# Kernel optimization log

Measured on AMD Instinct MI355X. Metric: run time of the kernel, lower is better.

Reference implementation:

```python
import jax, jax.numpy as jnp
import numpy as np

DIM = 768
H = 12          # num query heads
KV = 6          # num kv heads
GS = H // KV    # group size = 2
HD = DIM // H   # head dim = 64


def setup_inputs() -> dict:
    key = jax.random.key(0)
    ks = jax.random.split(key, 6)
    B, P = 8, 1024
    s = DIM ** -0.5
    x = jax.random.normal(ks[0], (B, P, DIM), dtype=jnp.float32)
    Wq = jax.random.normal(ks[1], (DIM, DIM), dtype=jnp.float32) * s
    Wk = jax.random.normal(ks[2], (DIM, KV * HD), dtype=jnp.float32) * s
    Wv = jax.random.normal(ks[3], (DIM, KV * HD), dtype=jnp.float32) * s
    Wp = jax.random.normal(ks[4], (DIM, DIM), dtype=jnp.float32) * s
    bp = jnp.zeros((DIM,), dtype=jnp.float32)
    return {"x": x, "Wq": Wq, "Wk": Wk, "Wv": Wv, "Wp": Wp, "bp": bp}


def reference(x, Wq, Wk, Wv, Wp, bp):
    B, P, C = x.shape
    scale = HD ** -0.5
    # projections; consecutive heads i*GS..(i+1)*GS-1 form kv-group i (torch.split dim=1)
    q = (x @ Wq).reshape(B, P, KV, GS, HD).transpose(0, 2, 3, 1, 4) * scale  # [B,KV,GS,P,d]
    k = (x @ Wk).reshape(B, P, KV, HD).transpose(0, 2, 1, 3)                 # [B,KV,P,d]
    v = (x @ Wv).reshape(B, P, KV, HD).transpose(0, 2, 1, 3)                 # [B,KV,P,d]

    scores = jnp.einsum('bghqd,bgkd->bghqk', q, k)      # [B,KV,GS,P,P]
    w = jax.nn.softmax(scores, axis=-1)                  # attn_drop=0 (eval)
    att = jnp.einsum('bghqk,bgkd->bghqd', w, v)          # [B,KV,GS,P,d]

    # per-group row-matched gaussian-ish noise (torch get_gaussian), vectorized over KV groups
    y = P * HD
    flat = att.reshape(B, KV, GS, y)                     # rows = groups within kv-group
    M = jax.random.uniform(jax.random.key(42), (KV, GS, y), dtype=flat.dtype)
    di = jnp.arange(min(GS, y))
    M = M.at[:, di, di].set(0.0)                         # sparse: zero diagonal
    m_mean = M.mean(axis=-1, keepdims=True)
    m_std = jnp.std(M, axis=-1, ddof=1, keepdims=True)   # torch.std is unbiased
    m_std = jnp.where(m_std == 0, jnp.ones_like(m_std), m_std)
    Z = (M - m_mean) / m_std                             # [KV,GS,y], shared across batch
    r_mean = flat.mean(axis=-1, keepdims=True)           # [B,KV,GS,1]
    r_std = jnp.std(flat, axis=-1, ddof=1, keepdims=True)
    flat = flat - (Z[None] * r_std + r_mean)

    att = flat.reshape(B, KV, GS, P, HD).reshape(B, H, P, HD)
    out = att.transpose(0, 2, 1, 3).reshape(B, P, C) @ Wp + bp  # proj_drop=0
    return out
```

## Files before the change

### kernel.cpp

```cpp
#include <hip/hip_runtime.h>
#include <hip/hip_bf16.h>
#include <math.h>


#define NTHREADS 256

typedef __bf16 bf16x8 __attribute__((ext_vector_type(8)));
typedef float f32x4 __attribute__((ext_vector_type(4)));

#define MFMA16(a, b, c) __builtin_amdgcn_mfma_f32_16x16x32_bf16(a, b, c, 0, 0, 0)

#define QSCALE 0.18033688011112042f

__device__ __forceinline__ float fexp2(float x) {
#if __has_builtin(__builtin_amdgcn_exp2f)
    return __builtin_amdgcn_exp2f(x);
#else
    return __expf(x * 0.6931471805599453f);
#endif
}

__device__ __forceinline__ void gload16(const void* g, void* l) {
    __builtin_amdgcn_global_load_lds(
        (const __attribute__((address_space(1))) void*)g,
        (__attribute__((address_space(3))) void*)l, 16, 0, 0);
}

__device__ __forceinline__ unsigned rotl_u32(unsigned x, int r) {
    return (x << r) | (x >> (32 - r));
}
__device__ __forceinline__ void threefry_0_42(unsigned x0, unsigned x1,
                                              unsigned& o0, unsigned& o1) {
    const unsigned ks0 = 0u, ks1 = 42u, ks2 = 0u ^ 42u ^ 0x1BD11BDAu;
    x0 += ks0; x1 += ks1;
#define R4(a,b,c,d) \
    x0 += x1; x1 = rotl_u32(x1,a); x1 ^= x0; \
    x0 += x1; x1 = rotl_u32(x1,b); x1 ^= x0; \
    x0 += x1; x1 = rotl_u32(x1,c); x1 ^= x0; \
    x0 += x1; x1 = rotl_u32(x1,d); x1 ^= x0;
    R4(13,15,26,6)   x0 += ks1; x1 += ks2 + 1u;
    R4(17,29,16,24)  x0 += ks2; x1 += ks0 + 2u;
    R4(13,15,26,6)   x0 += ks0; x1 += ks1 + 3u;
    R4(17,29,16,24)  x0 += ks1; x1 += ks2 + 4u;
    R4(13,15,26,6)   x0 += ks2; x1 += ks0 + 5u;
#undef R4
    o0 = x0; o1 = x1;
}
__device__ __forceinline__ float tf_uniform(unsigned i) {
    unsigned o0, o1;
    threefry_0_42(0u, i, o0, o1);
    unsigned bits = o0 ^ o1;
    return __uint_as_float((bits >> 9) | 0x3f800000u) - 1.0f;
}

__device__ __forceinline__ float wave_sum64(float v) {
#pragma unroll
    for (int off = 32; off; off >>= 1) v += __shfl_xor(v, off, 64);
    return v;
}

__device__ __forceinline__ unsigned short bf16_rne(float x) {
    unsigned u = __float_as_uint(x);
    return (unsigned short)((u + 0x7fffu + ((u >> 16) & 1u)) >> 16);
}
__device__ __forceinline__ unsigned pack_bf16x2(float lo, float hi) {
    return (unsigned)bf16_rne(lo) | ((unsigned)bf16_rne(hi) << 16);
}
__device__ __forceinline__ float bfu(unsigned v) {
    return __uint_as_float(v << 16);
}


__global__ __launch_bounds__(NTHREADS) void prep_k(
    const float* __restrict__ x, const float* __restrict__ Wq,
    const float* __restrict__ Wk, const float* __restrict__ Wv,
    const float* __restrict__ Wp,
    unsigned short* __restrict__ xb, unsigned short* __restrict__ wstk,
    unsigned short* __restrict__ wpt,
    unsigned short* __restrict__ zb, float* __restrict__ zpart)
{
    __shared__ float rbuf[8];
    int blk = blockIdx.x;
    if (blk < 1536) {
#pragma unroll
        for (int j = 0; j < 4; ++j) {
            int i = blk * 1024 + j * 256 + threadIdx.x;
            float4 v = ((const float4*)x)[i];
            uint2 u;
            u.x = pack_bf16x2(v.x, v.y);
            u.y = pack_bf16x2(v.z, v.w);
            int f0 = i * 4;
            int row = f0 / 768, col = f0 - row * 768;
            int kc = col >> 6, kin = col & 63;
            int kh = kin >> 5, g = (kin >> 3) & 3, e = col & 7;
            int chunk = row >> 4, cl = row & 15;
            size_t a = (((size_t)(kc * 512 + chunk)) * 2 + kh) * 512
                       + (g * 16 + cl) * 8 + e;
            *(uint2*)&xb[a] = u;
        }
    } else if (blk < 1920) {
        int zc = blk - 1536;
        int row = zc >> 5, chunk = zc & 31;
        int g = row & 1;
        int j0 = chunk * 2048;
        float sum = 0.f, sumsq = 0.f;
        for (int t = threadIdx.x; t < 2048; t += NTHREADS) {
            int j = j0 + t;
            unsigned i = (unsigned)row * 65536u + (unsigned)j;
            float m = tf_uniform(i);
            if (j == g) m = 0.f;
            zb[i] = bf16_rne(m);
            sum += m; sumsq += m * m;
        }
        sum = wave_sum64(sum); sumsq = wave_sum64(sumsq);
        int lane = threadIdx.x & 63, wv = threadIdx.x >> 6;
        if (lane == 0) { rbuf[wv] = sum; rbuf[4 + wv] = sumsq; }
        __syncthreads();
        if (threadIdx.x == 0) {
            zpart[zc * 2]     = rbuf[0] + rbuf[1] + rbuf[2] + rbuf[3];
            zpart[zc * 2 + 1] = rbuf[4] + rbuf[5] + rbuf[6] + rbuf[7];
        }
    } else {
        int id = blk - 1920;
        const float* W; unsigned short* dstbuf; int N, rowbase, NC;
        if (id < 144)      { W = Wq; dstbuf = wstk; N = 768; rowbase = 0;    NC = 96; }
        else if (id < 216) { W = Wk; dstbuf = wstk; N = 384; rowbase = 768;  NC = 96; id -= 144; }
        else if (id < 288) { W = Wv; dstbuf = wstk; N = 384; rowbase = 1152; NC = 96; id -= 216; }
        else               { W = Wp; dstbuf = wpt;  N = 768; rowbase = 0;    NC = 48; id -= 288; }
        int ntn = N >> 6;
        int kt = id / ntn, nt = id % ntn;
        int k0 = kt * 64, n0 = nt * 64;
        int t = threadIdx.x;
        int tn = t & 63, tk = t >> 6;
        float r[16];
#pragma unroll
        for (int j = 0; j < 16; ++j)
            r[j] = W[(size_t)(k0 + tk * 16 + j) * N + n0 + tn];
        uint4 u0, u1;
        u0.x = pack_bf16x2(r[0], r[1]);   u0.y = pack_bf16x2(r[2], r[3]);
        u0.z = pack_bf16x2(r[4], r[5]);   u0.w = pack_bf16x2(r[6], r[7]);
        u1.x = pack_bf16x2(r[8], r[9]);   u1.y = pack_bf16x2(r[10], r[11]);
        u1.z = pack_bf16x2(r[12], r[13]); u1.w = pack_bf16x2(r[14], r[15]);
        int rowg = rowbase + n0 + tn;
        int chunk = rowg >> 4, cl = rowg & 15;
        int kc = k0 >> 6;
        int kh = tk >> 1, g0 = (tk & 1) * 2;
        size_t base = (((size_t)(kc * NC + chunk)) * 2 + kh) * 512 + cl * 8;
        *(uint4*)&dstbuf[base + g0 * 128]       = u0;
        *(uint4*)&dstbuf[base + (g0 + 1) * 128] = u1;
    }
}

__device__ __forceinline__ void mfma_tile128x256(
    const unsigned short* __restrict__ Afb, int nca,
    const unsigned short* __restrict__ Bfb,
    int row0, int col0,
    unsigned short* As, unsigned short* Bs, f32x4 acc[4][4])
{
    const int tid = threadIdx.x;
    const int lane = tid & 63, w = tid >> 6;
    const int c = lane & 15, g = lane >> 4;
    const int wm = w & 1, wn = w >> 1;

#pragma unroll
    for (int mi = 0; mi < 4; ++mi)
#pragma unroll
        for (int ni = 0; ni < 4; ++ni) acc[mi][ni] = (f32x4){0.f, 0.f, 0.f, 0.f};

    const unsigned short* Abase = Afb + (size_t)(row0 >> 4) * 1024;
    const unsigned short* Bbase = Bfb + (size_t)(col0 >> 4) * 1024;

    for (int kc = 0; kc < 12; ++kc) {
        const unsigned short* a = Abase + (size_t)kc * nca * 1024;
        const unsigned short* bb = Bbase + (size_t)kc * 512 * 1024;
        __syncthreads();
        gload16(a  + tid * 8,         As + tid * 8);
        gload16(a  + tid * 8 + 4096,  As + tid * 8 + 4096);
        gload16(bb + tid * 8,         Bs + tid * 8);
        gload16(bb + tid * 8 + 4096,  Bs + tid * 8 + 4096);
        gload16(bb + tid * 8 + 8192,  Bs + tid * 8 + 8192);
        gload16(bb + tid * 8 + 12288, Bs + tid * 8 + 12288);
        __syncthreads();
#pragma unroll
        for (int ks = 0; ks < 2; ++ks) {
            bf16x8 aA[4], bB[4];
#pragma unroll
            for (int mi = 0; mi < 4; ++mi)
                aA[mi] = *(const bf16x8*)&As[(wm * 4 + mi) * 1024 + ks * 512 + g * 128 + c * 8];
#pragma unroll
            for (int ni = 0; ni < 4; ++ni)
                bB[ni] = *(const bf16x8*)&Bs[(wn * 4 + ni) * 1024 + ks * 512 + g * 128 + c * 8];
#pragma unroll
            for (int mi = 0; mi < 4; ++mi)
#pragma unroll
                for (int ni = 0; ni < 4; ++ni)
                    acc[mi][ni] = MFMA16(aA[mi], bB[ni], acc[mi][ni]);
        }
    }
}

__global__ __launch_bounds__(512) void qkv_mfma_k(
    const unsigned short* __restrict__ xb, const unsigned short* __restrict__ wstk,
    unsigned short* __restrict__ qbh, unsigned short* __restrict__ kb2,
    unsigned short* __restrict__ vb2)
{
    __shared__ unsigned short As[8192];
    __shared__ unsigned short Bs[16384];
    int id = blockIdx.x;
    int xcd = id & 7, slot = id >> 3;
    int col0i = xcd + ((slot & 3) << 3);
    int row0i = slot >> 2;
    int row0 = row0i * 128, col0 = col0i * 256;
    f32x4 acc[4][4];
    mfma_tile128x256(wstk, 96, xb, row0, col0, As, Bs, acc);

    const int tid = threadIdx.x;
    const int w = tid >> 6, lane = tid & 63;
    const int c = lane & 15, g = lane >> 4;
    const int wm = w & 1, wn = w >> 1;

#pragma unroll
    for (int mi = 0; mi < 4; ++mi) {
        int ocb = row0 + wm * 64 + mi * 16;
        int ocol = ocb + g * 4;
#pragma unroll
        for (int ni = 0; ni < 4; ++ni) {
            int pglob = col0 + wn * 64 + ni * 16 + c;
            int b = pglob >> 10, pin = pglob & 1023;
            if (ocb < 768) {
                ushort4 u;
                u.x = bf16_rne(acc[mi][ni][0] * QSCALE);
                u.y = bf16_rne(acc[mi][ni][1] * QSCALE);
                u.z = bf16_rne(acc[mi][ni][2] * QSCALE);
                u.w = bf16_rne(acc[mi][ni][3] * QSCALE);
                int h = ocol >> 6, d0 = ocol & 63;
                *(ushort4*)&qbh[(((size_t)b * 12 + h) * 1024 + pin) * 64 + d0] = u;
            } else if (ocb < 1152) {
                int kcol = ocol - 768;
                int kv = kcol >> 6, d0 = kcol & 63;
                int kt = pin >> 7, key = pin & 127;
                ushort4 u;
                u.x = bf16_rne(acc[mi][ni][0]);
                u.y = bf16_rne(acc[mi][ni][1]);
                u.z = bf16_rne(acc[mi][ni][2]);
                u.w = bf16_rne(acc[mi][ni][3]);
                *(ushort4*)&kb2[((((size_t)(b * 6 + kv) * 8 + kt) * 8 + (d0 >> 3)) * 128
                                 + key) * 8 + (d0 & 7)] = u;
            } else {
                int kt = pin >> 7, pg = (pin & 127) >> 3, p8 = pin & 7;
#pragma unroll
                for (int r = 0; r < 4; ++r) {
                    int vcol = ocol + r - 1152;
                    int kv = vcol >> 6, d = vcol & 63;
                    vb2[((((size_t)(b * 6 + kv) * 8 + kt) * 16 + pg) * 64 + d) * 8 + p8]
                        = bf16_rne(acc[mi][ni][r]);
                }
            }
        }
    }
}

__global__ __launch_bounds__(512) void proj_mfma_k(
    const unsigned short* __restrict__ attb, const unsigned short* __restrict__ wpt,
    const float* __restrict__ bp, float* __restrict__ out)
{
    __shared__ unsigned short As[8192];
    __shared__ unsigned short Bs[16384];
    int id = blockIdx.x;
    int xcd = id & 7, slot = id >> 3;
    int col0i = xcd + ((slot & 3) << 3);
    int row0i = slot >> 2;
    int row0 = row0i * 128, col0 = col0i * 256;
    f32x4 acc[4][4];
    mfma_tile128x256(wpt, 48, attb, row0, col0, As, Bs, acc);

    const int tid = threadIdx.x;
    const int w = tid >> 6, lane = tid & 63;
    const int c = lane & 15, g = lane >> 4;
    const int wm = w & 1, wn = w >> 1;
#pragma unroll
    for (int mi = 0; mi < 4; ++mi) {
        int ocol = row0 + wm * 64 + mi * 16 + g * 4;
        float4 bias = *(const float4*)&bp[ocol];
#pragma unroll
        for (int ni = 0; ni < 4; ++ni) {
            int p = col0 + wn * 64 + ni * 16 + c;
            float4 u;
            u.x = acc[mi][ni][0] + bias.x;
            u.y = acc[mi][ni][1] + bias.y;
            u.z = acc[mi][ni][2] + bias.z;
            u.w = acc[mi][ni][3] + bias.w;
            *(float4*)&out[(size_t)p * 768 + ocol] = u;
        }
    }
}

#define LDP 136
__global__ __launch_bounds__(NTHREADS) void attn_mfma_k(
    const unsigned short* __restrict__ qbh, const unsigned short* __restrict__ kb2,
    const unsigned short* __restrict__ vb2, unsigned short* __restrict__ attb,
    float* __restrict__ spart)
{
    __shared__ unsigned short P_lds[4 * 32 * LDP];
    __shared__ float l_s[4][32];
    __shared__ float sbuf[8];

    int id = blockIdx.x;
    int xcd = id & 7, slot = id >> 3;
    int grp = slot % 6, member = slot / 6;
    int g48 = xcd + 8 * grp;
    int b = g48 / 6, kv = g48 % 6;
    int h = kv * 2 + (member & 1);
    int qtile = member >> 1;
    const int qt0 = qtile * 128;

    const int tid = threadIdx.x;
    const int w = tid >> 6, lane = tid & 63;
    const int c = lane & 15, g = lane >> 4;

    const unsigned short* qh = qbh + (((size_t)b * 12 + h) * 1024 + qt0 + w * 32) * 64;
    const unsigned short* kbase = kb2 + ((size_t)(b * 6 + kv) * 8) * 8192;
    const unsigned short* vbase = vb2 + ((size_t)(b * 6 + kv) * 8) * 8192;
    unsigned short* Pw = P_lds + w * 32 * LDP;

    bf16x8 bQ[2][2];
#pragma unroll
    for (int ks = 0; ks < 2; ++ks) {
        bQ[ks][0] = *(const bf16x8*)(qh + (size_t)(c) * 64 + ks * 32 + g * 8);
        bQ[ks][1] = *(const bf16x8*)(qh + (size_t)(16 + c) * 64 + ks * 32 + g * 8);
    }

    f32x4 O[2][4];
#pragma unroll
    for (int i = 0; i < 2; ++i)
#pragma unroll
        for (int j = 0; j < 4; ++j) O[i][j] = (f32x4){0.f, 0.f, 0.f, 0.f};
    float l_r[2] = {0.f, 0.f};

    for (int t = 0; t < 8; ++t) {
        const unsigned short* kt = kbase + (size_t)t * 8192;
        const unsigned short* vt = vbase + (size_t)t * 8192;

        bf16x8 aK[2][8];
#pragma unroll
        for (int ks = 0; ks < 2; ++ks)
#pragma unroll
            for (int mb = 0; mb < 8; ++mb)
                aK[ks][mb] = *(const bf16x8*)(kt + ((size_t)(ks * 4 + g) * 128 + mb * 16 + c) * 8);

        f32x4 S[8][2];
#pragma unroll
        for (int mb = 0; mb < 8; ++mb) {
            S[mb][0] = (f32x4){0.f, 0.f, 0.f, 0.f};
            S[mb][1] = (f32x4){0.f, 0.f, 0.f, 0.f};
        }
#pragma unroll
        for (int ks = 0; ks < 2; ++ks)
#pragma unroll
            for (int mb = 0; mb < 8; ++mb) {
                S[mb][0] = MFMA16(aK[ks][mb], bQ[ks][0], S[mb][0]);
                S[mb][1] = MFMA16(aK[ks][mb], bQ[ks][1], S[mb][1]);
            }

        bf16x8 bV[4][4];
#pragma unroll
        for (int ks = 0; ks < 4; ++ks)
#pragma unroll
            for (int nb = 0; nb < 4; ++nb)
                bV[ks][nb] = *(const bf16x8*)(vt + ((size_t)(ks * 4 + g) * 64 + nb * 16 + c) * 8);

#pragma unroll
        for (int qn = 0; qn < 2; ++qn) {
            float lt = 0.f;
#pragma unroll
            for (int mb = 0; mb < 8; ++mb) {
                float p0 = fexp2(S[mb][qn][0]);
                float p1 = fexp2(S[mb][qn][1]);
                float p2 = fexp2(S[mb][qn][2]);
                float p3 = fexp2(S[mb][qn][3]);
                lt += (p0 + p1) + (p2 + p3);
                uint2 uu;
                uu.x = pack_bf16x2(p0, p1);
                uu.y = pack_bf16x2(p2, p3);
                *(uint2*)&Pw[(size_t)(qn * 16 + c) * LDP + mb * 16 + g * 4] = uu;
            }
            lt += __shfl_xor(lt, 16, 64);
            lt += __shfl_xor(lt, 32, 64);
            l_r[qn] += lt;
        }

#pragma unroll
        for (int ks = 0; ks < 4; ++ks) {
            bf16x8 aP0 = *(const bf16x8*)&Pw[(size_t)(c) * LDP + ks * 32 + g * 8];
            bf16x8 aP1 = *(const bf16x8*)&Pw[(size_t)(16 + c) * LDP + ks * 32 + g * 8];
#pragma unroll
            for (int nb = 0; nb < 4; ++nb) {
                O[0][nb] = MFMA16(aP0, bV[ks][nb], O[0][nb]);
                O[1][nb] = MFMA16(aP1, bV[ks][nb], O[1][nb]);
            }
        }
    }
    if (g == 0) { l_s[w][c] = l_r[0]; l_s[w][16 + c] = l_r[1]; }
    f32x4 li0 = *(f32x4*)&l_s[w][g * 4];
    f32x4 li1 = *(f32x4*)&l_s[w][16 + g * 4];
    float inv0[4], inv1[4];
#pragma unroll
    for (int r = 0; r < 4; ++r) { inv0[r] = 1.f / li0[r]; inv1[r] = 1.f / li1[r]; }
    int rowblk = (b * 1024 + qt0 + w * 32) >> 4;
    float psum = 0.f, psumsq = 0.f;
#pragma unroll
    for (int r = 0; r < 4; ++r) {
        int cl = g * 4 + r;
#pragma unroll
        for (int nb = 0; nb < 4; ++nb) {
            float o0 = O[0][nb][r] * inv0[r];
            float o1 = O[1][nb][r] * inv1[r];
            psum += o0 + o1;
            psumsq += o0 * o0 + o1 * o1;
            int kh = nb >> 1, gb = (nb & 1) * 2 + (c >> 3), e = c & 7;
            size_t a0 = (((size_t)h * 512 + rowblk) * 2 + kh) * 512
                        + (gb * 16 + cl) * 8 + e;
            size_t a1 = (((size_t)h * 512 + rowblk + 1) * 2 + kh) * 512
                        + (gb * 16 + cl) * 8 + e;
            attb[a0] = bf16_rne(o0);
            attb[a1] = bf16_rne(o1);
        }
    }
    psum = wave_sum64(psum); psumsq = wave_sum64(psumsq);
    if (lane == 0) { sbuf[w] = psum; sbuf[4 + w] = psumsq; }
    __syncthreads();
    if (tid == 0) {
        int idx = ((b * 12 + h) * 8 + qtile) * 2;
        spart[idx]     = sbuf[0] + sbuf[1] + sbuf[2] + sbuf[3];
        spart[idx + 1] = sbuf[4] + sbuf[5] + sbuf[6] + sbuf[7];
    }
}

__global__ __launch_bounds__(NTHREADS) void stats2_k(
    unsigned short* __restrict__ attb, const unsigned short* __restrict__ zb,
    const float* __restrict__ spart, const float* __restrict__ zpart)
{
    int blk = blockIdx.x;
    int bh = blk >> 3, ch = blk & 7;
    int b = bh / 12, h = bh % 12;
    float zs = 0.f, zs2 = 0.f, rs = 0.f, rs2 = 0.f;
#pragma unroll
    for (int cc = 0; cc < 32; ++cc) {
        zs  += zpart[(h * 32 + cc) * 2];
        zs2 += zpart[(h * 32 + cc) * 2 + 1];
    }
#pragma unroll
    for (int cc = 0; cc < 8; ++cc) {
        rs  += spart[(bh * 8 + cc) * 2];
        rs2 += spart[(bh * 8 + cc) * 2 + 1];
    }
    float m_mean = zs * (1.f / 65536.f);
    float m_var  = (zs2 - 65536.f * m_mean * m_mean) * (1.f / 65535.f);
    float m_sd   = sqrtf(fmaxf(m_var, 0.f));
    if (m_sd == 0.f) m_sd = 1.f;
    float r_mean = rs * (1.f / 65536.f);
    float r_var  = (rs2 - 65536.f * r_mean * r_mean) * (1.f / 65535.f);
    float r_sd   = sqrtf(fmaxf(r_var, 0.f));
    float a = r_sd / m_sd;
    float bc = m_mean * a - r_mean;

    const unsigned short* zrow = zb + (size_t)h * 65536 + (size_t)ch * 8192;
    for (int f = threadIdx.x; f < 1024; f += NTHREADS) {
        int p = f >> 3, dq = (f & 7) * 8;
        int row = b * 1024 + ch * 128 + p;
        int chunk = row >> 4, cl = row & 15;
        int kh = dq >> 5, gb = (dq >> 3) & 3;
        size_t aoff = (((size_t)h * 512 + chunk) * 2 + kh) * 512 + (gb * 16 + cl) * 8;
        unsigned short* ptr = attb + aoff;
        uint4 u = *(const uint4*)ptr;
        uint4 zu = *(const uint4*)(zrow + (size_t)f * 8);
        float v0 = bfu(u.x)       - bfu(zu.x)       * a + bc;
        float v1 = bfu(u.x >> 16) - bfu(zu.x >> 16) * a + bc;
        float v2 = bfu(u.y)       - bfu(zu.y)       * a + bc;
        float v3 = bfu(u.y >> 16) - bfu(zu.y >> 16) * a + bc;
        float v4 = bfu(u.z)       - bfu(zu.z)       * a + bc;
        float v5 = bfu(u.z >> 16) - bfu(zu.z >> 16) * a + bc;
        float v6 = bfu(u.w)       - bfu(zu.w)       * a + bc;
        float v7 = bfu(u.w >> 16) - bfu(zu.w >> 16) * a + bc;
        uint4 o;
        o.x = pack_bf16x2(v0, v1);
        o.y = pack_bf16x2(v2, v3);
        o.z = pack_bf16x2(v4, v5);
        o.w = pack_bf16x2(v6, v7);
        *(uint4*)ptr = o;
    }
}

extern "C" void kernel_launch(void* const* d_in, const int* in_sizes, int n_in,
                              void* d_out, int out_size, void* d_ws, size_t ws_size,
                              hipStream_t stream) {
    const float* x  = (const float*)d_in[0];
    const float* Wq = (const float*)d_in[1];
    const float* Wk = (const float*)d_in[2];
    const float* Wv = (const float*)d_in[3];
    const float* Wp = (const float*)d_in[4];
    const float* bp = (const float*)d_in[5];
    float* out = (float*)d_out;

    float* ws    = (float*)d_ws;
    float* zpart = ws;
    float* spart = zpart + 768;
    unsigned short* zb   = (unsigned short*)(spart + 1536);
    unsigned short* xb   = zb + 786432;
    unsigned short* wstk = xb + 6291456;
    unsigned short* wpt  = wstk + 1179648;
    unsigned short* qbh  = wpt + 589824;
    unsigned short* kb2  = qbh + 6291456;
    unsigned short* vb2  = kb2 + 3145728;
    unsigned short* attb = vb2 + 3145728;

    prep_k<<<2352, NTHREADS, 0, stream>>>(x, Wq, Wk, Wv, Wp,
                                          xb, wstk, wpt, zb, zpart);
    qkv_mfma_k<<<384, 512, 0, stream>>>(xb, wstk, qbh, kb2, vb2);
    attn_mfma_k<<<768, NTHREADS, 0, stream>>>(qbh, kb2, vb2, attb, spart);
    stats2_k<<<768, NTHREADS, 0, stream>>>(attb, zb, spart, zpart);
    proj_mfma_k<<<192, 512, 0, stream>>>(attb, wpt, bp, out);
}
```

Baseline: 188.7 us.

## Split attention KV range across wave pairs and double block count

Each attention block now covers 64 query rows instead of 128, and its four waves split as two query groups times two halves of the key range. Partial O and row sums from the second key half are combined through LDS before normalization. The grid doubles to 1536 blocks, stats partials double to 16 per head, and the per-qn P tile shrinks so LDS use per block drops. The bf16 pack now uses a byte-permute instruction. The intent is more parallelism and occupancy, at the cost of an LDS reduction, extra syncs, and each K/V tile being loaded by twice as many blocks.

```diff
diff --git a/kernel.cpp b/kernel.cpp
--- a/kernel.cpp
+++ b/kernel.cpp
@@ -64,7 +64,10 @@
     return (unsigned short)((u + 0x7fffu + ((u >> 16) & 1u)) >> 16);
 }
 __device__ __forceinline__ unsigned pack_bf16x2(float lo, float hi) {
-    return (unsigned)bf16_rne(lo) | ((unsigned)bf16_rne(hi) << 16);
+    unsigned ul = __float_as_uint(lo), uh = __float_as_uint(hi);
+    unsigned rl = ul + 0x7fffu + ((ul >> 16) & 1u);
+    unsigned rh = uh + 0x7fffu + ((uh >> 16) & 1u);
+    return __builtin_amdgcn_perm(rh, rl, 0x07060302u);
 }
 __device__ __forceinline__ float bfu(unsigned v) {
     return __uint_as_float(v << 16);
@@ -301,8 +304,9 @@
     const unsigned short* __restrict__ vb2, unsigned short* __restrict__ attb,
     float* __restrict__ spart)
 {
-    __shared__ unsigned short P_lds[4 * 32 * LDP];
-    __shared__ float l_s[4][32];
+    __shared__ unsigned short P_lds[4 * 16 * LDP];
+    __shared__ float lx[2][64][2];
+    __shared__ float l_s[2][32];
     __shared__ float sbuf[8];
 
     int id = blockIdx.x;
@@ -311,17 +315,18 @@
     int g48 = xcd + 8 * grp;
     int b = g48 / 6, kv = g48 % 6;
     int h = kv * 2 + (member & 1);
-    int qtile = member >> 1;
-    const int qt0 = qtile * 128;
+    int qt64 = member >> 1;
+    const int qt0 = qt64 * 64;
 
     const int tid = threadIdx.x;
     const int w = tid >> 6, lane = tid & 63;
     const int c = lane & 15, g = lane >> 4;
-
-    const unsigned short* qh = qbh + (((size_t)b * 12 + h) * 1024 + qt0 + w * 32) * 64;
+    const int qg = w & 1, kg = w >> 1;
+
+    const unsigned short* qh = qbh + (((size_t)b * 12 + h) * 1024 + qt0 + qg * 32) * 64;
     const unsigned short* kbase = kb2 + ((size_t)(b * 6 + kv) * 8) * 8192;
     const unsigned short* vbase = vb2 + ((size_t)(b * 6 + kv) * 8) * 8192;
-    unsigned short* Pw = P_lds + w * 32 * LDP;
+    unsigned short* Pw = P_lds + w * 16 * LDP;
 
     bf16x8 bQ[2][2];
 #pragma unroll
@@ -337,7 +342,9 @@
         for (int j = 0; j < 4; ++j) O[i][j] = (f32x4){0.f, 0.f, 0.f, 0.f};
     float l_r[2] = {0.f, 0.f};
 
-    for (int t = 0; t < 8; ++t) {
+#pragma unroll 1
+    for (int tt = 0; tt < 4; ++tt) {
+        int t = kg * 4 + tt;
         const unsigned short* kt = kbase + (size_t)t * 8192;
         const unsigned short* vt = vbase + (size_t)t * 8192;
 
@@ -382,57 +389,78 @@
                 uint2 uu;
                 uu.x = pack_bf16x2(p0, p1);
                 uu.y = pack_bf16x2(p2, p3);
-                *(uint2*)&Pw[(size_t)(qn * 16 + c) * LDP + mb * 16 + g * 4] = uu;
+                *(uint2*)&Pw[(size_t)c * LDP + mb * 16 + g * 4] = uu;
             }
             lt += __shfl_xor(lt, 16, 64);
             lt += __shfl_xor(lt, 32, 64);
             l_r[qn] += lt;
-        }
-
-#pragma unroll
-        for (int ks = 0; ks < 4; ++ks) {
-            bf16x8 aP0 = *(const bf16x8*)&Pw[(size_t)(c) * LDP + ks * 32 + g * 8];
-            bf16x8 aP1 = *(const bf16x8*)&Pw[(size_t)(16 + c) * LDP + ks * 32 + g * 8];
+#pragma unroll
+            for (int ks = 0; ks < 4; ++ks) {
+                bf16x8 aP = *(const bf16x8*)&Pw[(size_t)c * LDP + ks * 32 + g * 8];
+#pragma unroll
+                for (int nb = 0; nb < 4; ++nb)
+                    O[qn][nb] = MFMA16(aP, bV[ks][nb], O[qn][nb]);
+            }
+        }
+    }
+
+    __syncthreads();
+    float* comb = (float*)P_lds;
+    if (w >= 2) {
+        int base = ((w - 2) * 64 + lane) * 32;
+#pragma unroll
+        for (int qn = 0; qn < 2; ++qn)
+#pragma unroll
+            for (int nb = 0; nb < 4; ++nb)
+                *(f32x4*)&comb[base + qn * 16 + nb * 4] = O[qn][nb];
+        lx[w - 2][lane][0] = l_r[0];
+        lx[w - 2][lane][1] = l_r[1];
+    }
+    __syncthreads();
+    if (w < 2) {
+        int base = (w * 64 + lane) * 32;
+#pragma unroll
+        for (int qn = 0; qn < 2; ++qn)
+#pragma unroll
+            for (int nb = 0; nb < 4; ++nb)
+                O[qn][nb] += *(f32x4*)&comb[base + qn * 16 + nb * 4];
+        l_r[0] += lx[w][lane][0];
+        l_r[1] += lx[w][lane][1];
+
+        if (g == 0) { l_s[w][c] = l_r[0]; l_s[w][16 + c] = l_r[1]; }
+        f32x4 li0 = *(f32x4*)&l_s[w][g * 4];
+        f32x4 li1 = *(f32x4*)&l_s[w][16 + g * 4];
+        float inv0[4], inv1[4];
+#pragma unroll
+        for (int r = 0; r < 4; ++r) { inv0[r] = 1.f / li0[r]; inv1[r] = 1.f / li1[r]; }
+        int rowblk = (b * 1024 + qt0 + w * 32) >> 4;
+        float psum = 0.f, psumsq = 0.f;
+#pragma unroll
+        for (int r = 0; r < 4; ++r) {
+            int cl = g * 4 + r;
 #pragma unroll
             for (int nb = 0; nb < 4; ++nb) {
-                O[0][nb] = MFMA16(aP0, bV[ks][nb], O[0][nb]);
-                O[1][nb] = MFMA16(aP1, bV[ks][nb], O[1][nb]);
+                float o0 = O[0][nb][r] * inv0[r];
+                float o1 = O[1][nb][r] * inv1[r];
+                psum += o0 + o1;
+                psumsq += o0 * o0 + o1 * o1;
+                int kh = nb >> 1, gb = (nb & 1) * 2 + (c >> 3), e = c & 7;
+                size_t a0 = (((size_t)h * 512 + rowblk) * 2 + kh) * 512
+                            + (gb * 16 + cl) * 8 + e;
+                size_t a1 = (((size_t)h * 512 + rowblk + 1) * 2 + kh) * 512
+                            + (gb * 16 + cl) * 8 + e;
+                attb[a0] = bf16_rne(o0);
+                attb[a1] = bf16_rne(o1);
             }
         }
-    }
-    if (g == 0) { l_s[w][c] = l_r[0]; l_s[w][16 + c] = l_r[1]; }
-    f32x4 li0 = *(f32x4*)&l_s[w][g * 4];
-    f32x4 li1 = *(f32x4*)&l_s[w][16 + g * 4];
-    float inv0[4], inv1[4];
-#pragma unroll
-    for (int r = 0; r < 4; ++r) { inv0[r] = 1.f / li0[r]; inv1[r] = 1.f / li1[r]; }
-    int rowblk = (b * 1024 + qt0 + w * 32) >> 4;
-    float psum = 0.f, psumsq = 0.f;
-#pragma unroll
-    for (int r = 0; r < 4; ++r) {
-        int cl = g * 4 + r;
-#pragma unroll
-        for (int nb = 0; nb < 4; ++nb) {
-            float o0 = O[0][nb][r] * inv0[r];
-            float o1 = O[1][nb][r] * inv1[r];
-            psum += o0 + o1;
-            psumsq += o0 * o0 + o1 * o1;
-            int kh = nb >> 1, gb = (nb & 1) * 2 + (c >> 3), e = c & 7;
-            size_t a0 = (((size_t)h * 512 + rowblk) * 2 + kh) * 512
-                        + (gb * 16 + cl) * 8 + e;
-            size_t a1 = (((size_t)h * 512 + rowblk + 1) * 2 + kh) * 512
-                        + (gb * 16 + cl) * 8 + e;
-            attb[a0] = bf16_rne(o0);
-            attb[a1] = bf16_rne(o1);
-        }
-    }
-    psum = wave_sum64(psum); psumsq = wave_sum64(psumsq);
-    if (lane == 0) { sbuf[w] = psum; sbuf[4 + w] = psumsq; }
+        psum = wave_sum64(psum); psumsq = wave_sum64(psumsq);
+        if (lane == 0) { sbuf[w] = psum; sbuf[4 + w] = psumsq; }
+    }
     __syncthreads();
     if (tid == 0) {
-        int idx = ((b * 12 + h) * 8 + qtile) * 2;
-        spart[idx]     = sbuf[0] + sbuf[1] + sbuf[2] + sbuf[3];
-        spart[idx + 1] = sbuf[4] + sbuf[5] + sbuf[6] + sbuf[7];
+        int idx = ((b * 12 + h) * 16 + qt64) * 2;
+        spart[idx]     = sbuf[0] + sbuf[1];
+        spart[idx + 1] = sbuf[4] + sbuf[5];
     }
 }
 
@@ -450,9 +478,9 @@
         zs2 += zpart[(h * 32 + cc) * 2 + 1];
     }
 #pragma unroll
-    for (int cc = 0; cc < 8; ++cc) {
-        rs  += spart[(bh * 8 + cc) * 2];
-        rs2 += spart[(bh * 8 + cc) * 2 + 1];
+    for (int cc = 0; cc < 16; ++cc) {
+        rs  += spart[(bh * 16 + cc) * 2];
+        rs2 += spart[(bh * 16 + cc) * 2 + 1];
     }
     float m_mean = zs * (1.f / 65536.f);
     float m_var  = (zs2 - 65536.f * m_mean * m_mean) * (1.f / 65535.f);
@@ -505,7 +533,7 @@
     float* ws    = (float*)d_ws;
     float* zpart = ws;
     float* spart = zpart + 768;
-    unsigned short* zb   = (unsigned short*)(spart + 1536);
+    unsigned short* zb   = (unsigned short*)(spart + 3072);
     unsigned short* xb   = zb + 786432;
     unsigned short* wstk = xb + 6291456;
     unsigned short* wpt  = wstk + 1179648;
@@ -517,7 +545,7 @@
     prep_k<<<2352, NTHREADS, 0, stream>>>(x, Wq, Wk, Wv, Wp,
                                           xb, wstk, wpt, zb, zpart);
     qkv_mfma_k<<<384, 512, 0, stream>>>(xb, wstk, qbh, kb2, vb2);
-    attn_mfma_k<<<768, NTHREADS, 0, stream>>>(qbh, kb2, vb2, attb, spart);
+    attn_mfma_k<<<1536, NTHREADS, 0, stream>>>(qbh, kb2, vb2, attb, spart);
     stats2_k<<<768, NTHREADS, 0, stream>>>(attb, zb, spart, zpart);
     proj_mfma_k<<<192, 512, 0, stream>>>(attb, wpt, bp, out);
 }
```

New measurement: 209.8 us. 11.2% more time.
